# Performance work log

Measured on AMD Instinct MI355X. Metric: run time of the kernel, lower is better.

The kernel has to match this reference:

```python
import jax, jax.numpy as jnp
import numpy as np

N_HEADS = 16
HEAD_DIM = 64
ROPE_THETA = 10000.0


def rotate_half(x):
    x1, x2 = jnp.split(x, 2, axis=-1)
    return jnp.concatenate([-x2, x1], axis=-1)


def setup_inputs() -> dict:
    key = jax.random.key(0)
    k0, k1, k2 = jax.random.split(key, 3)
    B, L, C = 2, 2048, 1024
    x = jax.random.normal(k0, (B, L, C), dtype=jnp.float32)
    # causal additive bias, as used by VAR-style blockwise masks (here full causal)
    causal = jnp.tril(jnp.ones((L, L), dtype=bool))
    attn_bias = jnp.where(causal, 0.0, -1e9).astype(jnp.float32)[None, None]
    position_ids = jnp.broadcast_to(jnp.arange(L, dtype=jnp.int32), (B, L))
    qkv_w = 0.02 * jax.random.normal(k1, (3 * C, C), dtype=jnp.float32)
    q_bias = jnp.zeros((C,), jnp.float32)
    v_bias = jnp.zeros((C,), jnp.float32)
    proj_w = 0.02 * jax.random.normal(k2, (C, C), dtype=jnp.float32)
    proj_b = jnp.zeros((C,), jnp.float32)
    return {"x": x, "attn_bias": attn_bias, "position_ids": position_ids,
            "qkv_w": qkv_w, "q_bias": q_bias, "v_bias": v_bias,
            "proj_w": proj_w, "proj_b": proj_b}


def reference(x, attn_bias, position_ids, qkv_w, q_bias, v_bias, proj_w, proj_b):
    B, L, C = x.shape
    H, D = N_HEADS, HEAD_DIM
    # fused QKV projection with concatenated (q_bias, 0, v_bias)
    bias = jnp.concatenate([q_bias, jnp.zeros_like(q_bias), v_bias])
    qkv = (jnp.einsum('blc,oc->blo', x, qkv_w) + bias).reshape(B, L, 3, H, D)
    q = jnp.transpose(qkv[:, :, 0], (0, 2, 1, 3))  # [B,H,L,D]
    k = jnp.transpose(qkv[:, :, 1], (0, 2, 1, 3))
    v = jnp.transpose(qkv[:, :, 2], (0, 2, 1, 3))
    # Llama rotary embedding: cos/sin [B,L,D] -> unsqueeze dim=1
    inv_freq = 1.0 / (ROPE_THETA ** (jnp.arange(0, D, 2, dtype=jnp.float32) / D))
    freqs = position_ids.astype(jnp.float32)[:, :, None] * inv_freq  # [B,L,D/2]
    emb = jnp.concatenate([freqs, freqs], axis=-1)
    cos = jnp.cos(emb)[:, None]  # [B,1,L,D]
    sin = jnp.sin(emb)[:, None]
    q = q * cos + rotate_half(q) * sin
    k = k * cos + rotate_half(k) * sin
    # slow_attn: (q*scale) @ k^T + bias -> softmax -> @ v
    scale = 0.25 / np.sqrt(D).astype(np.float32)
    attn = jnp.einsum('bhqd,bhkd->bhqk', q * scale, k) + attn_bias
    attn = jax.nn.softmax(attn, axis=-1)
    out = jnp.einsum('bhqk,bhkd->bhqd', attn, v)
    out = out.transpose(0, 2, 1, 3).reshape(B, L, C)
    return jnp.einsum('blc,oc->blo', out, proj_w) + proj_b
```

## Files before the change

kernel.cpp:

```cpp
#include <hip/hip_runtime.h>

typedef unsigned short u16;
typedef unsigned int u32;
typedef __attribute__((ext_vector_type(8))) short short8;
typedef __attribute__((ext_vector_type(4))) float f32x4;
typedef __attribute__((ext_vector_type(2))) unsigned int u32x2;
typedef __attribute__((ext_vector_type(4))) unsigned short u16x4;
typedef __attribute__((ext_vector_type(8))) unsigned short u16x8;

#define AS1 __attribute__((address_space(1)))
#define AS3 __attribute__((address_space(3)))

__device__ __forceinline__ u16 f2bf(float f) {
  u32 u = __builtin_bit_cast(u32, f);
  u32 r = u + 0x7FFFu + ((u >> 16) & 1u);
  return (u16)(r >> 16);
}
__device__ __forceinline__ float bf2f(u16 h) {
  u32 u = ((u32)h) << 16;
  return __builtin_bit_cast(float, u);
}
__device__ __forceinline__ void gload_lds16(const void* g, void* l) {
  __builtin_amdgcn_global_load_lds((AS1 void*)g, (AS3 void*)l, 16, 0, 0);
}
__device__ __forceinline__ float fexp2(float x) {
  float r;
  asm("v_exp_f32 %0, %1" : "=v"(r) : "v"(x));
  return r;
}

#define QSCALE 0.04508422002778011f

__device__ __forceinline__ void cvt_body(const float* __restrict__ src, u16* __restrict__ dst,
                                         int i) {
  float4 v = ((const float4*)src)[i];
  u16x4 o;
  o[0] = f2bf(v.x); o[1] = f2bf(v.y); o[2] = f2bf(v.z); o[3] = f2bf(v.w);
  ((u16x4*)dst)[i] = o;
}

__global__ __launch_bounds__(256)
void pre_kernel(const float* __restrict__ x, const float* __restrict__ w1,
                const float* __restrict__ w2, const int* __restrict__ pos,
                u16* __restrict__ x_bf, u16* __restrict__ w1_bf, u16* __restrict__ w2_bf,
                float* __restrict__ tab) {
  int bid = blockIdx.x;
  int t = threadIdx.x;
  if (bid < 4096) {
    cvt_body(x, x_bf, bid * 256 + t);
  } else if (bid < 7168) {
    cvt_body(w1, w1_bf, (bid - 4096) * 256 + t);
  } else if (bid < 8192) {
    cvt_body(w2, w2_bf, (bid - 7168) * 256 + t);
  } else {
    int idx = (bid - 8192) * 256 + t;
    int i = idx & 31;
    int bl = idx >> 5;
    float p = (float)pos[bl];
    float inv_freq = 1.0f / powf(10000.0f, (2.0f * (float)i) / 64.0f);
    float ang = p * inv_freq;
    tab[(size_t)bl * 64 + i] = cosf(ang);
    tab[(size_t)bl * 64 + 32 + i] = sinf(ang);
  }
}

template <bool OUT_BF16>
__global__ __launch_bounds__(256)
void gemm_bt_kernel(const u16* __restrict__ A, const u16* __restrict__ Bw,
                    void* __restrict__ Cout, const float* __restrict__ bias,
                    int M, int N, int K, int NXT) {
  __shared__ alignas(16) u16 As[128 * 64];
  __shared__ alignas(16) u16 Bs[128 * 64];
  const int tid = threadIdx.x;
  const int lane = tid & 63, wave = tid >> 6;
  const int wr = wave >> 1, wc = wave & 1;
  const int nblk = gridDim.x;
  const int lin = (blockIdx.x & 7) * (nblk >> 3) + (blockIdx.x >> 3);
  const int m0 = (lin / NXT) * 128, n0 = (lin % NXT) * 128;
  const int r = lane & 15, g = lane >> 4;

  f32x4 acc[4][4] = {};

  const int nk = K >> 6;
  for (int kt = 0; kt < nk; ++kt) {
    const int k0 = kt << 6;
#pragma unroll
    for (int c = 0; c < 4; ++c) {
      int i = c * 256 + tid;
      int row = i >> 3, slot = i & 7;
      int ss = slot ^ (row & 7);
      const u16* gA = A + (size_t)(m0 + row) * K + k0 + ss * 8;
      const u16* gB = Bw + (size_t)(n0 + row) * K + k0 + ss * 8;
      void* lA = (char*)As + c * 4096 + wave * 1024;
      void* lB = (char*)Bs + c * 4096 + wave * 1024;
      gload_lds16(gA, lA);
      gload_lds16(gB, lB);
    }
    __syncthreads();
#pragma unroll
    for (int kk = 0; kk < 2; ++kk) {
      short8 af[4], bf[4];
#pragma unroll
      for (int m = 0; m < 4; ++m) {
        int row = wr * 64 + m * 16 + r;
        int byte = row * 128 + (((kk * 4 + g) ^ (row & 7)) << 4);
        af[m] = *(const short8*)((const char*)As + byte);
      }
#pragma unroll
      for (int n = 0; n < 4; ++n) {
        int row = wc * 64 + n * 16 + r;
        int byte = row * 128 + (((kk * 4 + g) ^ (row & 7)) << 4);
        bf[n] = *(const short8*)((const char*)Bs + byte);
      }
#pragma unroll
      for (int m = 0; m < 4; ++m)
#pragma unroll
        for (int n = 0; n < 4; ++n)
          acc[m][n] = __builtin_amdgcn_mfma_f32_16x16x32_bf16(af[m], bf[n], acc[m][n], 0, 0, 0);
    }
    __syncthreads();
  }

  if constexpr (OUT_BF16) {
    u16* C = (u16*)Cout;
#pragma unroll
    for (int m = 0; m < 4; ++m) {
      int rg = m0 + wr * 64 + m * 16 + g * 4;
#pragma unroll
      for (int n = 0; n < 4; ++n) {
        int cg = n0 + wc * 64 + n * 16 + r;
#pragma unroll
        for (int j = 0; j < 4; ++j)
          C[(size_t)(rg + j) * N + cg] = f2bf(acc[m][n][j]);
      }
    }
  } else {
    float* C = (float*)Cout;
#pragma unroll
    for (int m = 0; m < 4; ++m) {
      int rg = m0 + wr * 64 + m * 16 + g * 4;
#pragma unroll
      for (int n = 0; n < 4; ++n) {
        int cg = n0 + wc * 64 + n * 16 + r;
        float bv = bias[cg];
#pragma unroll
        for (int j = 0; j < 4; ++j)
          C[(size_t)(rg + j) * N + cg] = acc[m][n][j] + bv;
      }
    }
  }
}

__global__ __launch_bounds__(256)
void gemm_bt64_kernel(const u16* __restrict__ A, const u16* __restrict__ Bw,
                      float* __restrict__ Cout, const float* __restrict__ bias,
                      int M, int N, int K, int NXT) {
  __shared__ alignas(16) u16 As[128 * 64];
  __shared__ alignas(16) u16 Bs[64 * 64];
  const int tid = threadIdx.x;
  const int lane = tid & 63, wave = tid >> 6;
  const int wr = wave >> 1, wc = wave & 1;
  const int nblk = gridDim.x;
  const int lin = (blockIdx.x & 7) * (nblk >> 3) + (blockIdx.x >> 3);
  const int m0 = (lin / NXT) * 128, n0 = (lin % NXT) * 64;
  const int r = lane & 15, g = lane >> 4;

  f32x4 acc[4][2] = {};

  const int nk = K >> 6;
  for (int kt = 0; kt < nk; ++kt) {
    const int k0 = kt << 6;
#pragma unroll
    for (int c = 0; c < 4; ++c) {
      int i = c * 256 + tid;
      int row = i >> 3, slot = i & 7;
      int ss = slot ^ (row & 7);
      const u16* gA = A + (size_t)(m0 + row) * K + k0 + ss * 8;
      void* lA = (char*)As + c * 4096 + wave * 1024;
      gload_lds16(gA, lA);
    }
#pragma unroll
    for (int c = 0; c < 2; ++c) {
      int i = c * 256 + tid;
      int row = i >> 3, slot = i & 7;
      int ss = slot ^ (row & 7);
      const u16* gB = Bw + (size_t)(n0 + row) * K + k0 + ss * 8;
      void* lB = (char*)Bs + c * 4096 + wave * 1024;
      gload_lds16(gB, lB);
    }
    __syncthreads();
#pragma unroll
    for (int kk = 0; kk < 2; ++kk) {
      short8 af[4], bf[2];
#pragma unroll
      for (int m = 0; m < 4; ++m) {
        int row = wr * 64 + m * 16 + r;
        int byte = row * 128 + (((kk * 4 + g) ^ (row & 7)) << 4);
        af[m] = *(const short8*)((const char*)As + byte);
      }
#pragma unroll
      for (int n = 0; n < 2; ++n) {
        int row = wc * 32 + n * 16 + r;
        int byte = row * 128 + (((kk * 4 + g) ^ (row & 7)) << 4);
        bf[n] = *(const short8*)((const char*)Bs + byte);
      }
#pragma unroll
      for (int m = 0; m < 4; ++m)
#pragma unroll
        for (int n = 0; n < 2; ++n)
          acc[m][n] = __builtin_amdgcn_mfma_f32_16x16x32_bf16(af[m], bf[n], acc[m][n], 0, 0, 0);
    }
    __syncthreads();
  }

#pragma unroll
  for (int m = 0; m < 4; ++m) {
    int rg = m0 + wr * 64 + m * 16 + g * 4;
#pragma unroll
    for (int n = 0; n < 2; ++n) {
      int cg = n0 + wc * 32 + n * 16 + r;
      float bv = bias[cg];
#pragma unroll
      for (int j = 0; j < 4; ++j)
        Cout[(size_t)(rg + j) * N + cg] = acc[m][n][j] + bv;
    }
  }
}

__global__ __launch_bounds__(256)
void mid_kernel(const u16* __restrict__ qkv, const float* __restrict__ tab,
                const float* __restrict__ q_bias, const float* __restrict__ v_bias,
                u16* __restrict__ Qo, u16* __restrict__ Ko, u16* __restrict__ vt) {
  __shared__ alignas(16) u16 tile[64][72];
  int bid = blockIdx.x;
  int t = threadIdx.x;
  if (bid < 4096) {
    int bl = bid;
    int b = bl >> 11, l = bl & 2047;
    const float* tr = tab + (size_t)bl * 64;
    const u16* base = qkv + (size_t)bl * 3072;
#pragma unroll
    for (int pp = 0; pp < 2; ++pp) {
      int p = t + pp * 256;
      int h = p >> 5, d = p & 31;
      float c = tr[d], s = tr[32 + d];
      size_t o = ((size_t)(b * 16 + h) * 2048 + l) * 64 + d;
      float x1 = bf2f(base[h * 64 + d]) + q_bias[h * 64 + d];
      float x2 = bf2f(base[h * 64 + d + 32]) + q_bias[h * 64 + d + 32];
      Qo[o]      = f2bf((x1 * c - x2 * s) * QSCALE);
      Qo[o + 32] = f2bf((x2 * c + x1 * s) * QSCALE);
      x1 = bf2f(base[1024 + h * 64 + d]);
      x2 = bf2f(base[1024 + h * 64 + d + 32]);
      Ko[o]      = f2bf(x1 * c - x2 * s);
      Ko[o + 32] = f2bf(x2 * c + x1 * s);
    }
  } else {
    int bid2 = bid - 4096;
    int bh = bid2 >> 5;
    int b = bh >> 4, h = bh & 15;
    int l0 = (bid2 & 31) * 64;
    int rr = t >> 2;
    int c0 = (t & 3) * 16;
    const u16* src = qkv + ((size_t)(b * 2048 + l0 + rr)) * 3072 + 2048 + h * 64 + c0;
    u16x8 a = *(const u16x8*)src;
    u16x8 bb = *(const u16x8*)(src + 8);
#pragma unroll
    for (int i = 0; i < 8; ++i) {
      a[i]  = f2bf(bf2f(a[i])  + v_bias[h * 64 + c0 + i]);
      bb[i] = f2bf(bf2f(bb[i]) + v_bias[h * 64 + c0 + 8 + i]);
    }
    *(u16x8*)&tile[rr][c0] = a;
    *(u16x8*)&tile[rr][c0 + 8] = bb;
    __syncthreads();
    int d = t >> 2;
    int lc = (t & 3) * 16;
    u16x8 o1, o2;
#pragma unroll
    for (int i = 0; i < 8; ++i) {
      o1[i] = tile[lc + i][d];
      o2[i] = tile[lc + 8 + i][d];
    }
    u16* dst = vt + ((size_t)bh * 64 + d) * 2048 + l0 + lc;
    *(u16x8*)dst = o1;
    *(u16x8*)(dst + 8) = o2;
  }
}

__global__ __launch_bounds__(512)
void attn_kernel(const u16* __restrict__ Q, const u16* __restrict__ Kmat,
                 const u16* __restrict__ Vt, u16* __restrict__ O) {
  __shared__ alignas(16) u16 Ks[4][64 * 64];
  __shared__ alignas(16) u16 Vs[4][64 * 64];
  __shared__ alignas(16) u16 Pbuf[8][1024];
  const int tid = threadIdx.x;
  const int lane = tid & 63;
  const int wave = tid >> 6;
  const int id = blockIdx.x;
  const int xcd = id & 7, rank = id >> 3;
  const int bh = xcd + 8 * (rank & 3);
  const int xqA = 31 - (rank >> 2);
  const int wt = wave >> 2;
  const int xq = wt ? (xqA - 16) : xqA;
  const int ntA = xqA + 1;
  const int nt = xq + 1;
  const int b = bh >> 4, h = bh & 15;
  const int r = lane & 15, g = lane >> 4;

  const u16* Kb = Kmat + (size_t)bh * 2048 * 64;
  const u16* Vb = Vt + (size_t)bh * 64 * 2048;

  const int srow = wave * 8 + (lane >> 3);
  const int sslot = (lane & 7) ^ (srow & 7);

#define STAGE(tt, bb) do { \
    gload_lds16(Kb + ((size_t)((tt) * 64 + srow)) * 64 + sslot * 8, \
                (char*)Ks[bb] + wave * 1024); \
    gload_lds16(Vb + (size_t)srow * 2048 + (tt) * 64 + sslot * 8, \
                (char*)Vs[bb] + wave * 1024); \
  } while (0)

  u16* Pw = Pbuf[wave];
  const int qrow0 = xq * 64 + (wave & 3) * 16;
  const u16* Qb = Q + ((size_t)bh * 2048 + qrow0) * 64;

  short8 qf[2];
#pragma unroll
  for (int kk = 0; kk < 2; ++kk)
    qf[kk] = *(const short8*)(Qb + r * 64 + kk * 32 + g * 8);

  short8 ones;
#pragma unroll
  for (int i = 0; i < 8; ++i) ones[i] = (short)0x3F80;

  f32x4 o_acc[4] = {};
  f32x4 l_acc = {};

  STAGE(0, 0);
  STAGE(1, 1);
  asm volatile("s_waitcnt vmcnt(0)" ::: "memory");
  __builtin_amdgcn_s_barrier();

  const int nss = (ntA + 1) >> 1;
  for (int ss = 0; ss < nss; ++ss) {
    const int t0 = 2 * ss, t1 = t0 + 1;
    const int cb = 2 * (ss & 1);
    const int sb = 2 * ((ss + 1) & 1);

    if (t0 + 2 < ntA) STAGE(t0 + 2, sb);
    if (t0 + 3 < ntA) STAGE(t0 + 3, sb + 1);

    const bool a0 = (t0 < nt);
    const bool a1 = (t1 < nt);

    f32x4 s0[4] = {}, s1[4] = {};
    __builtin_amdgcn_s_setprio(1);
    if (a0) {
      const char* Kc = (const char*)Ks[cb];
#pragma unroll
      for (int ct = 0; ct < 4; ++ct)
#pragma unroll
        for (int kk = 0; kk < 2; ++kk) {
          int row = ct * 16 + r;
          int byte = row * 128 + (((kk * 4 + g) ^ (row & 7)) << 4);
          short8 kf = *(const short8*)(Kc + byte);
          s0[ct] = __builtin_amdgcn_mfma_f32_16x16x32_bf16(kf, qf[kk], s0[ct], 0, 0, 0);
        }
    }
    if (a1) {
      const char* Kc = (const char*)Ks[cb + 1];
#pragma unroll
      for (int ct = 0; ct < 4; ++ct)
#pragma unroll
        for (int kk = 0; kk < 2; ++kk) {
          int row = ct * 16 + r;
          int byte = row * 128 + (((kk * 4 + g) ^ (row & 7)) << 4);
          short8 kf = *(const short8*)(Kc + byte);
          s1[ct] = __builtin_amdgcn_mfma_f32_16x16x32_bf16(kf, qf[kk], s1[ct], 0, 0, 0);
        }
    }
    __builtin_amdgcn_s_setprio(0);

    if (a0 && t0 * 64 + 63 > qrow0) {
      int qrow = qrow0 + r;
#pragma unroll
      for (int ct = 0; ct < 4; ++ct)
#pragma unroll
        for (int j = 0; j < 4; ++j) {
          int kv = t0 * 64 + ct * 16 + 4 * g + j;
          if (kv > qrow) s0[ct][j] = -1e30f;
        }
    }
    if (a1 && t1 * 64 + 63 > qrow0) {
      int qrow = qrow0 + r;
#pragma unroll
      for (int ct = 0; ct < 4; ++ct)
#pragma unroll
        for (int j = 0; j < 4; ++j) {
          int kv = t1 * 64 + ct * 16 + 4 * g + j;
          if (kv > qrow) s1[ct][j] = -1e30f;
        }
    }

    u32x2 pk0[4], pk1[4];
    if (a0) {
#pragma unroll
      for (int ct = 0; ct < 4; ++ct) {
        float p0 = fexp2(s0[ct][0]);
        float p1 = fexp2(s0[ct][1]);
        float p2 = fexp2(s0[ct][2]);
        float p3 = fexp2(s0[ct][3]);
        asm("v_cvt_pk_bf16_f32 %0, %1, %2" : "=v"(pk0[ct][0]) : "v"(p0), "v"(p1));
        asm("v_cvt_pk_bf16_f32 %0, %1, %2" : "=v"(pk0[ct][1]) : "v"(p2), "v"(p3));
      }
    }
    if (a1) {
#pragma unroll
      for (int ct = 0; ct < 4; ++ct) {
        float p0 = fexp2(s1[ct][0]);
        float p1 = fexp2(s1[ct][1]);
        float p2 = fexp2(s1[ct][2]);
        float p3 = fexp2(s1[ct][3]);
        asm("v_cvt_pk_bf16_f32 %0, %1, %2" : "=v"(pk1[ct][0]) : "v"(p0), "v"(p1));
        asm("v_cvt_pk_bf16_f32 %0, %1, %2" : "=v"(pk1[ct][1]) : "v"(p2), "v"(p3));
      }
    }

    if (a0) {
#pragma unroll
      for (int ct = 0; ct < 4; ++ct) {
        int byte = r * 128 + ((32 * ct + 8 * g) ^ ((r & 7) << 4));
        *(u32x2*)((char*)Pw + byte) = pk0[ct];
      }
      const char* Vc = (const char*)Vs[cb];
      __builtin_amdgcn_s_setprio(1);
#pragma unroll
      for (int kk = 0; kk < 2; ++kk) {
        int byte = r * 128 + (((kk * 4 + g) ^ (r & 7)) << 4);
        short8 pf = *(const short8*)((const char*)Pw + byte);
        l_acc = __builtin_amdgcn_mfma_f32_16x16x32_bf16(pf, ones, l_acc, 0, 0, 0);
#pragma unroll
        for (int n = 0; n < 4; ++n) {
          int row = n * 16 + r;
          int vbyte = row * 128 + (((kk * 4 + g) ^ (row & 7)) << 4);
          short8 vf = *(const short8*)(Vc + vbyte);
          o_acc[n] = __builtin_amdgcn_mfma_f32_16x16x32_bf16(pf, vf, o_acc[n], 0, 0, 0);
        }
      }
      __builtin_amdgcn_s_setprio(0);
    }

    if (a1) {
#pragma unroll
      for (int ct = 0; ct < 4; ++ct) {
        int byte = r * 128 + ((32 * ct + 8 * g) ^ ((r & 7) << 4));
        *(u32x2*)((char*)Pw + byte) = pk1[ct];
      }
      const char* Vc = (const char*)Vs[cb + 1];
      __builtin_amdgcn_s_setprio(1);
#pragma unroll
      for (int kk = 0; kk < 2; ++kk) {
        int byte = r * 128 + (((kk * 4 + g) ^ (r & 7)) << 4);
        short8 pf = *(const short8*)((const char*)Pw + byte);
        l_acc = __builtin_amdgcn_mfma_f32_16x16x32_bf16(pf, ones, l_acc, 0, 0, 0);
#pragma unroll
        for (int n = 0; n < 4; ++n) {
          int row = n * 16 + r;
          int vbyte = row * 128 + (((kk * 4 + g) ^ (row & 7)) << 4);
          short8 vf = *(const short8*)(Vc + vbyte);
          o_acc[n] = __builtin_amdgcn_mfma_f32_16x16x32_bf16(pf, vf, o_acc[n], 0, 0, 0);
        }
      }
      __builtin_amdgcn_s_setprio(0);
    }

    if (ss + 1 < nss) {
      asm volatile("s_waitcnt vmcnt(0)" ::: "memory");
      __builtin_amdgcn_s_barrier();
    }
  }
#undef STAGE

  float ij[4];
#pragma unroll
  for (int j = 0; j < 4; ++j) ij[j] = 1.0f / l_acc[j];
#pragma unroll
  for (int n = 0; n < 4; ++n)
#pragma unroll
    for (int j = 0; j < 4; ++j) {
      size_t idx = ((size_t)b * 2048 + qrow0 + 4 * g + j) * 1024 + h * 64 + n * 16 + r;
      O[idx] = f2bf(o_acc[n][j] * ij[j]);
    }
}

extern "C" void kernel_launch(void* const* d_in, const int* in_sizes, int n_in,
                              void* d_out, int out_size, void* d_ws, size_t ws_size,
                              hipStream_t stream) {
  const float* x      = (const float*)d_in[0];
  const int*   pos    = (const int*)d_in[2];
  const float* qkv_w  = (const float*)d_in[3];
  const float* q_bias = (const float*)d_in[4];
  const float* v_bias = (const float*)d_in[5];
  const float* proj_w = (const float*)d_in[6];
  const float* proj_b = (const float*)d_in[7];
  float* out = (float*)d_out;

  char* ws = (char*)d_ws;
  u16* x_bf    = (u16*)(ws + 0);
  u16* w1_bf   = (u16*)(ws + 8388608);
  u16* w2_bf   = (u16*)(ws + 14680064);
  u16* qkv_bf  = (u16*)(ws + 16777216);
  u16* q_bf    = (u16*)(ws + 41943040);
  u16* k_bf    = (u16*)(ws + 50331648);
  u16* vt_bf   = (u16*)(ws + 58720256);
  u16* attn_bf = (u16*)(ws + 67108864);
  float* tab   = (float*)(ws + 75497472);

  pre_kernel<<<8704, 256, 0, stream>>>(x, qkv_w, proj_w, pos, x_bf, w1_bf, w2_bf, tab);
  gemm_bt_kernel<true><<<768, 256, 0, stream>>>(x_bf, w1_bf, qkv_bf, nullptr,
                                                4096, 3072, 1024, 24);
  mid_kernel<<<5120, 256, 0, stream>>>(qkv_bf, tab, q_bias, v_bias, q_bf, k_bf, vt_bf);
  attn_kernel<<<512, 512, 0, stream>>>(q_bf, k_bf, vt_bf, attn_bf);
  gemm_bt64_kernel<<<512, 256, 0, stream>>>(attn_bf, w2_bf, out, proj_b,
                                            4096, 1024, 1024, 16);
}
```

Baseline: 110.3 us.

## Replace QKV GEMM with 256x256 double-buffered 512-thread kernel

The QKV projection GEMM moves from 128x128 tiles with 256 threads and a single LDS buffer to 256x256 tiles with 8 waves and double-buffered LDS. Loads for the next k-tile are issued while MFMAs run on the current one, and s_setprio raises wave priority around the MFMA bursts. The aim is to hide global-to-LDS latency, halve barrier count, and raise data reuse per loaded byte. In exchange the grid shrinks to 192 blocks on a 256-CU device, which leaves CUs idle, and the 128 KB LDS footprint allows only one block per CU.

```diff
diff --git a/kernel.cpp b/kernel.cpp
--- a/kernel.cpp
+++ b/kernel.cpp
@@ -64,89 +64,92 @@
   }
 }
 
-template <bool OUT_BF16>
-__global__ __launch_bounds__(256)
-void gemm_bt_kernel(const u16* __restrict__ A, const u16* __restrict__ Bw,
-                    void* __restrict__ Cout, const float* __restrict__ bias,
-                    int M, int N, int K, int NXT) {
-  __shared__ alignas(16) u16 As[128 * 64];
-  __shared__ alignas(16) u16 Bs[128 * 64];
+__global__ __launch_bounds__(512)
+void gemm256_kernel(const u16* __restrict__ A, const u16* __restrict__ Bw,
+                    u16* __restrict__ C, int M, int N, int K, int NXT) {
+  __shared__ alignas(16) u16 Abuf[2][256 * 64];
+  __shared__ alignas(16) u16 Bbuf[2][256 * 64];
   const int tid = threadIdx.x;
   const int lane = tid & 63, wave = tid >> 6;
-  const int wr = wave >> 1, wc = wave & 1;
-  const int nblk = gridDim.x;
-  const int lin = (blockIdx.x & 7) * (nblk >> 3) + (blockIdx.x >> 3);
-  const int m0 = (lin / NXT) * 128, n0 = (lin % NXT) * 128;
+  const int wm = wave >> 2, wn = wave & 3;
+  const int lin = (blockIdx.x & 7) * (gridDim.x >> 3) + (blockIdx.x >> 3);
+  const int m0 = (lin / NXT) * 256, n0 = (lin % NXT) * 256;
   const int r = lane & 15, g = lane >> 4;
 
-  f32x4 acc[4][4] = {};
-
+  const int srow_base = tid >> 3;
+  const int sslot = tid & 7;
+
+  f32x4 acc[8][4] = {};
   const int nk = K >> 6;
+
+#define STAGE_C(kt_, d_, c_) do { \
+    int row_ = (c_) * 64 + srow_base; \
+    int ss_ = sslot ^ (row_ & 7); \
+    gload_lds16(A + (size_t)(m0 + row_) * K + ((kt_) << 6) + ss_ * 8, \
+                (char*)Abuf[d_] + (c_) * 8192 + wave * 1024); \
+    gload_lds16(Bw + (size_t)(n0 + row_) * K + ((kt_) << 6) + ss_ * 8, \
+                (char*)Bbuf[d_] + (c_) * 8192 + wave * 1024); \
+  } while (0)
+
+  STAGE_C(0, 0, 0); STAGE_C(0, 0, 1); STAGE_C(0, 0, 2); STAGE_C(0, 0, 3);
+  asm volatile("s_waitcnt vmcnt(0)" ::: "memory");
+  __builtin_amdgcn_s_barrier();
+
   for (int kt = 0; kt < nk; ++kt) {
-    const int k0 = kt << 6;
-#pragma unroll
-    for (int c = 0; c < 4; ++c) {
-      int i = c * 256 + tid;
-      int row = i >> 3, slot = i & 7;
-      int ss = slot ^ (row & 7);
-      const u16* gA = A + (size_t)(m0 + row) * K + k0 + ss * 8;
-      const u16* gB = Bw + (size_t)(n0 + row) * K + k0 + ss * 8;
-      void* lA = (char*)As + c * 4096 + wave * 1024;
-      void* lB = (char*)Bs + c * 4096 + wave * 1024;
-      gload_lds16(gA, lA);
-      gload_lds16(gB, lB);
-    }
-    __syncthreads();
-#pragma unroll
-    for (int kk = 0; kk < 2; ++kk) {
-      short8 af[4], bf[4];
-#pragma unroll
-      for (int m = 0; m < 4; ++m) {
-        int row = wr * 64 + m * 16 + r;
-        int byte = row * 128 + (((kk * 4 + g) ^ (row & 7)) << 4);
-        af[m] = *(const short8*)((const char*)As + byte);
-      }
-#pragma unroll
-      for (int n = 0; n < 4; ++n) {
-        int row = wc * 64 + n * 16 + r;
-        int byte = row * 128 + (((kk * 4 + g) ^ (row & 7)) << 4);
-        bf[n] = *(const short8*)((const char*)Bs + byte);
-      }
-#pragma unroll
-      for (int m = 0; m < 4; ++m)
-#pragma unroll
-        for (int n = 0; n < 4; ++n)
-          acc[m][n] = __builtin_amdgcn_mfma_f32_16x16x32_bf16(af[m], bf[n], acc[m][n], 0, 0, 0);
-    }
-    __syncthreads();
-  }
-
-  if constexpr (OUT_BF16) {
-    u16* C = (u16*)Cout;
-#pragma unroll
-    for (int m = 0; m < 4; ++m) {
-      int rg = m0 + wr * 64 + m * 16 + g * 4;
-#pragma unroll
-      for (int n = 0; n < 4; ++n) {
-        int cg = n0 + wc * 64 + n * 16 + r;
-#pragma unroll
-        for (int j = 0; j < 4; ++j)
-          C[(size_t)(rg + j) * N + cg] = f2bf(acc[m][n][j]);
-      }
-    }
-  } else {
-    float* C = (float*)Cout;
-#pragma unroll
-    for (int m = 0; m < 4; ++m) {
-      int rg = m0 + wr * 64 + m * 16 + g * 4;
-#pragma unroll
-      for (int n = 0; n < 4; ++n) {
-        int cg = n0 + wc * 64 + n * 16 + r;
-        float bv = bias[cg];
-#pragma unroll
-        for (int j = 0; j < 4; ++j)
-          C[(size_t)(rg + j) * N + cg] = acc[m][n][j] + bv;
-      }
+    const int d = kt & 1;
+    const char* Ac = (const char*)Abuf[d];
+    const char* Bc = (const char*)Bbuf[d];
+#pragma unroll
+    for (int p = 0; p < 4; ++p) {
+      if (p < 2 && kt + 1 < nk) {
+        STAGE_C(kt + 1, d ^ 1, 2 * p);
+        STAGE_C(kt + 1, d ^ 1, 2 * p + 1);
+      }
+      const int mq = p >> 1, nq = p & 1;
+      short8 af[4][2], bfr[2][2];
+#pragma unroll
+      for (int ml = 0; ml < 4; ++ml)
+#pragma unroll
+        for (int kk = 0; kk < 2; ++kk) {
+          int row = wm * 128 + (mq * 4 + ml) * 16 + r;
+          af[ml][kk] = *(const short8*)(Ac + row * 128 + (((kk * 4 + g) ^ (row & 7)) << 4));
+        }
+#pragma unroll
+      for (int nl = 0; nl < 2; ++nl)
+#pragma unroll
+        for (int kk = 0; kk < 2; ++kk) {
+          int row = wn * 64 + (nq * 2 + nl) * 16 + r;
+          bfr[nl][kk] = *(const short8*)(Bc + row * 128 + (((kk * 4 + g) ^ (row & 7)) << 4));
+        }
+      __builtin_amdgcn_s_setprio(1);
+#pragma unroll
+      for (int ml = 0; ml < 4; ++ml)
+#pragma unroll
+        for (int nl = 0; nl < 2; ++nl)
+#pragma unroll
+          for (int kk = 0; kk < 2; ++kk)
+            acc[mq * 4 + ml][nq * 2 + nl] =
+                __builtin_amdgcn_mfma_f32_16x16x32_bf16(af[ml][kk], bfr[nl][kk],
+                                                        acc[mq * 4 + ml][nq * 2 + nl],
+                                                        0, 0, 0);
+      __builtin_amdgcn_s_setprio(0);
+    }
+    if (kt + 1 < nk) {
+      asm volatile("s_waitcnt vmcnt(0)" ::: "memory");
+      __builtin_amdgcn_s_barrier();
+    }
+  }
+#undef STAGE_C
+
+#pragma unroll
+  for (int m = 0; m < 8; ++m) {
+    int rg = m0 + wm * 128 + m * 16 + g * 4;
+#pragma unroll
+    for (int n = 0; n < 4; ++n) {
+      int cg = n0 + wn * 64 + n * 16 + r;
+#pragma unroll
+      for (int j = 0; j < 4; ++j)
+        C[(size_t)(rg + j) * N + cg] = f2bf(acc[m][n][j]);
     }
   }
 }
@@ -516,8 +519,7 @@
   float* tab   = (float*)(ws + 75497472);
 
   pre_kernel<<<8704, 256, 0, stream>>>(x, qkv_w, proj_w, pos, x_bf, w1_bf, w2_bf, tab);
-  gemm_bt_kernel<true><<<768, 256, 0, stream>>>(x_bf, w1_bf, qkv_bf, nullptr,
-                                                4096, 3072, 1024, 24);
+  gemm256_kernel<<<192, 512, 0, stream>>>(x_bf, w1_bf, qkv_bf, 4096, 3072, 1024, 12);
   mid_kernel<<<5120, 256, 0, stream>>>(qkv_bf, tab, q_bias, v_bias, q_bf, k_bf, vt_bf);
   attn_kernel<<<512, 512, 0, stream>>>(q_bf, k_bf, vt_bf, attn_bf);
   gemm_bt64_kernel<<<512, 256, 0, stream>>>(attn_bf, w2_bf, out, proj_b,
```

New measurement: 117.0 us. 1.06x slower.
